# Kernel optimization log

Measured on AMD Instinct MI355X. Metric: run time of the kernel, lower is better.

The kernel has to match this reference:

```python
import jax, jax.numpy as jnp
import numpy as np


def setup_inputs() -> dict:
    key = jax.random.key(0)
    k1, k2 = jax.random.split(key)
    B, S_ENC, S_DEC, D = 8, 2048, 2048, 1024
    enc_outputs = jax.random.normal(k1, (B, S_ENC, D), dtype=jnp.float32)
    dec_outputs = jax.random.normal(k2, (B, S_DEC, D), dtype=jnp.float32)
    return {"enc_outputs": enc_outputs, "dec_outputs": dec_outputs}


def reference(enc_outputs, dec_outputs):
    # scores: [B, S_enc, S_dec] = enc @ dec^T (unscaled)
    a_t = jnp.einsum('bed,btd->bet', enc_outputs, dec_outputs)
    a_t = jax.nn.softmax(a_t, axis=-1)
    # context: [B, S_dec, D] = a_t^T @ enc
    c_t = jnp.einsum('bet,bed->btd', a_t, enc_outputs)
    return c_t
```

## Files before the change

### kernel.cpp

```cpp
#include <hip/hip_runtime.h>


typedef _Float16 half8 __attribute__((ext_vector_type(8)));
typedef _Float16 half4v __attribute__((ext_vector_type(4)));
typedef float floatx16 __attribute__((ext_vector_type(16)));

#define BM 128
#define BN 128
#define BK 32

__device__ __forceinline__ void async_load16(const _Float16* g, void* l) {
  __builtin_amdgcn_global_load_lds(
      (const __attribute__((address_space(1))) void*)g,
      (__attribute__((address_space(3))) void*)l, 16, 0, 0);
}

template <typename OutT, int RN>
__global__ __launch_bounds__(256, 2) void gemm_bt(
    const _Float16* __restrict__ A, const _Float16* __restrict__ Bt,
    OutT* __restrict__ C, int K, long strideA, long strideB, long strideC,
    int ldA, int ldB, int ldC) {
  __shared__ _Float16 lds_a[BM * BK];
  __shared__ _Float16 lds_b[BN * BK];

  const int b = blockIdx.z;
  A += (long)b * strideA;
  Bt += (long)b * strideB;
  C += (long)b * strideC;

  const int id = blockIdx.y * gridDim.x + blockIdx.x;
  const int xcd = id & 7;
  const int l = id >> 3;
  const int by = (xcd & 3) * 4 + l / RN;
  const int bx = (xcd >> 2) * RN + l % RN;
  const int m0 = by * BM;
  const int n0 = bx * BN;

  const int tid = threadIdx.x;
  const int lane = tid & 63;
  const int wave = tid >> 6;
  const int l31 = lane & 31;
  const int kh = lane >> 5;
  const int wm = (wave >> 1) * 64;
  const int wn = (wave & 1) * 64;

  floatx16 acc[2][2] = {};

  for (int k0 = 0; k0 < K; k0 += BK) {
#pragma unroll
    for (int c = 0; c < 2; ++c) {
      const int off = c * 4096 + wave * 1024 + lane * 16;
      const int row = off >> 6;
      const int ke = (((off >> 4) & 3) ^ (row & 3)) * 8;
      async_load16(A + (long)(m0 + row) * ldA + k0 + ke, (char*)lds_a + off);
      async_load16(Bt + (long)(n0 + row) * ldB + k0 + ke, (char*)lds_b + off);
    }
    __syncthreads();

    half8 af[2][2], bf[2][2];
#pragma unroll
    for (int i = 0; i < 2; ++i) {
      const int ra = wm + i * 32 + l31;
      const int rb = wn + i * 32 + l31;
#pragma unroll
      for (int s = 0; s < 2; ++s) {
        const int ck = s * 2 + kh;
        af[i][s] = *(const half8*)((const char*)lds_a + ra * 64 +
                                   ((ck ^ (ra & 3)) << 4));
        bf[i][s] = *(const half8*)((const char*)lds_b + rb * 64 +
                                   ((ck ^ (rb & 3)) << 4));
      }
    }
#pragma unroll
    for (int s = 0; s < 2; ++s)
#pragma unroll
      for (int i = 0; i < 2; ++i)
#pragma unroll
        for (int j = 0; j < 2; ++j)
          acc[i][j] = __builtin_amdgcn_mfma_f32_32x32x16_f16(
              af[i][s], bf[j][s], acc[i][j], 0, 0, 0);
    __syncthreads();
  }

#pragma unroll
  for (int i = 0; i < 2; ++i) {
    const int r_base = m0 + wm + i * 32 + 4 * kh;
#pragma unroll
    for (int j = 0; j < 2; ++j) {
      const int col = n0 + wn + j * 32 + l31;
#pragma unroll
      for (int g = 0; g < 4; ++g)
#pragma unroll
        for (int rr = 0; rr < 4; ++rr)
          C[(long)(r_base + g * 8 + rr) * ldC + col] =
              (OutT)acc[i][j][g * 4 + rr];
    }
  }
}

__global__ __launch_bounds__(256) void conv_enc(const float* __restrict__ E,
                                                _Float16* __restrict__ Eh,
                                                _Float16* __restrict__ EhT,
                                                int Se, int D) {
  __shared__ _Float16 T[64][72];
  const int b = blockIdx.z;
  const int d0 = blockIdx.x * 64;
  const int e0 = blockIdx.y * 64;
  const float* Eb = E + (size_t)b * Se * D;
  _Float16* Ehb = Eh + (size_t)b * Se * D;
  _Float16* EhTb = EhT + (size_t)b * D * Se;
  const int tid = threadIdx.x;
  const int tx = tid & 15;
  const int ty = tid >> 4;

  half4v h[4];
#pragma unroll
  for (int r = 0; r < 4; ++r) {
    const int e = e0 + ty * 4 + r;
    float4 v = *(const float4*)(Eb + (size_t)e * D + d0 + tx * 4);
    h[r][0] = (_Float16)v.x; h[r][1] = (_Float16)v.y;
    h[r][2] = (_Float16)v.z; h[r][3] = (_Float16)v.w;
    *(half4v*)(Ehb + (size_t)e * D + d0 + tx * 4) = h[r];
  }
#pragma unroll
  for (int c = 0; c < 4; ++c) {
    half4v w;
#pragma unroll
    for (int r = 0; r < 4; ++r) w[r] = h[r][c];
    *(half4v*)&T[tx * 4 + c][ty * 4] = w;
  }
  __syncthreads();
#pragma unroll
  for (int p = 0; p < 2; ++p) {
    const int idx = tid + p * 256;
    const int row = idx >> 3;
    const int ck = idx & 7;
    *(half8*)(EhTb + (size_t)(d0 + row) * Se + e0 + ck * 8) =
        *(const half8*)&T[row][ck * 8];
  }
}

__global__ __launch_bounds__(256) void conv_dec(const float* __restrict__ X,
                                                _Float16* __restrict__ Y) {
  const size_t i = ((size_t)blockIdx.x * 256 + threadIdx.x) * 8;
  float4 a = *(const float4*)(X + i);
  float4 b = *(const float4*)(X + i + 4);
  half8 h;
  h[0] = (_Float16)a.x; h[1] = (_Float16)a.y;
  h[2] = (_Float16)a.z; h[3] = (_Float16)a.w;
  h[4] = (_Float16)b.x; h[5] = (_Float16)b.y;
  h[6] = (_Float16)b.z; h[7] = (_Float16)b.w;
  *(half8*)(Y + i) = h;
}

__global__ __launch_bounds__(256) void row_stats(const _Float16* __restrict__ S,
                                                 float2* __restrict__ stats) {
  const int lane = threadIdx.x & 63;
  const long row = (long)blockIdx.x * 4 + (threadIdx.x >> 6);
  const _Float16* p = S + row * 2048;

  float f[32];
#pragma unroll
  for (int q = 0; q < 4; ++q) {
    half8 v = *(const half8*)(p + q * 512 + lane * 8);
#pragma unroll
    for (int j = 0; j < 8; ++j) f[q * 8 + j] = (float)v[j];
  }
  float mx = f[0];
#pragma unroll
  for (int j = 1; j < 32; ++j) mx = fmaxf(mx, f[j]);
  for (int o = 32; o; o >>= 1) mx = fmaxf(mx, __shfl_xor(mx, o, 64));
  float s = 0.f;
#pragma unroll
  for (int j = 0; j < 32; ++j) s += __expf(f[j] - mx);
  for (int o = 32; o; o >>= 1) s += __shfl_xor(s, o, 64);
  if (lane == 0) stats[row] = make_float2(mx, 1.0f / s);
}

__global__ __launch_bounds__(256) void norm_transpose(
    const _Float16* __restrict__ S, const float2* __restrict__ stats,
    _Float16* __restrict__ PT, int Se, int St) {
  __shared__ _Float16 T[64][72];
  const int b = blockIdx.z;
  const int t0 = blockIdx.x * 64;
  const int e0 = blockIdx.y * 64;
  const _Float16* Sb = S + (size_t)b * Se * St;
  _Float16* Pb = PT + (size_t)b * St * Se;
  const float2* stb = stats + (size_t)b * Se;
  const int tid = threadIdx.x;
  const int tx = tid & 15;
  const int ty = tid >> 4;

  half4v pr[4];
#pragma unroll
  for (int r = 0; r < 4; ++r) {
    const int e = e0 + ty * 4 + r;
    const float2 st = stb[e];
    half4v v = *(const half4v*)(Sb + (size_t)e * St + t0 + tx * 4);
#pragma unroll
    for (int c = 0; c < 4; ++c)
      pr[r][c] = (_Float16)(__expf((float)v[c] - st.x) * st.y);
  }
#pragma unroll
  for (int c = 0; c < 4; ++c) {
    half4v w;
#pragma unroll
    for (int r = 0; r < 4; ++r) w[r] = pr[r][c];
    *(half4v*)&T[tx * 4 + c][ty * 4] = w;
  }
  __syncthreads();
#pragma unroll
  for (int p = 0; p < 2; ++p) {
    const int idx = tid + p * 256;
    const int row = idx >> 3;
    const int ck = idx & 7;
    *(half8*)(Pb + (size_t)(t0 + row) * Se + e0 + ck * 8) =
        *(const half8*)&T[row][ck * 8];
  }
}

extern "C" void kernel_launch(void* const* d_in, const int* in_sizes, int n_in,
                              void* d_out, int out_size, void* d_ws,
                              size_t ws_size, hipStream_t stream) {
  const float* enc = (const float*)d_in[0];
  const float* dec = (const float*)d_in[1];
  float* out = (float*)d_out;

  const int B = 8, SE = 2048, SD = 2048, D = 1024;
  char* ws = (char*)d_ws;
  _Float16* enc_h = (_Float16*)ws;
  _Float16* dec_h = (_Float16*)(ws + 33554432);
  _Float16* PT = (_Float16*)ws;
  _Float16* enc_hT = (_Float16*)(ws + 67108864);
  _Float16* S_h = (_Float16*)(ws + 100663296);
  float2* stats = (float2*)(ws + 167772160);

  conv_enc<<<dim3(D / 64, SE / 64, B), 256, 0, stream>>>(enc, enc_h, enc_hT,
                                                         SE, D);
  conv_dec<<<dim3((size_t)B * SD * D / 2048), 256, 0, stream>>>(dec, dec_h);
  gemm_bt<_Float16, 8><<<dim3(SD / BN, SE / BM, B), 256, 0, stream>>>(
      enc_h, dec_h, S_h, D, (long)SE * D, (long)SD * D, (long)SE * SD, D, D,
      SD);
  row_stats<<<dim3(B * SE / 4), 256, 0, stream>>>(S_h, stats);
  norm_transpose<<<dim3(SD / 64, SE / 64, B), 256, 0, stream>>>(S_h, stats, PT,
                                                                SE, SD);
  gemm_bt<float, 4><<<dim3(D / BN, SD / BM, B), 256, 0, stream>>>(
      PT, enc_hT, out, SE, (long)SD * SE, (long)D * SE, (long)SD * D, SE, SE,
      D);
}
```

Baseline: 376.2 us.

## Emit transposed scores from GEMM epilogue, column-wise softmax stats, double GEMM BK

The first GEMM now writes the score matrix transposed through an LDS-staged epilogue, so the softmax normalization becomes a coalesced streaming pass instead of a separate transpose kernel. Softmax statistics are computed column-wise over the transposed layout with online max/sum partials, then merged in a small combine kernel. The GEMM K-tile grows from 32 to 64, halving loop iterations and barriers at the cost of more LDS per block, which may reduce occupancy. One extra kernel launch is added and the column-stat reads are narrower than the old row reads.

After: 349.9 us. 1.08x faster.

```diff
diff --git a/kernel.cpp b/kernel.cpp
--- a/kernel.cpp
+++ b/kernel.cpp
@@ -7,7 +7,7 @@
 
 #define BM 128
 #define BN 128
-#define BK 32
+#define BK 64
 
 __device__ __forceinline__ void async_load16(const _Float16* g, void* l) {
   __builtin_amdgcn_global_load_lds(
@@ -15,13 +15,16 @@
       (__attribute__((address_space(3))) void*)l, 16, 0, 0);
 }
 
-template <typename OutT, int RN>
+template <typename OutT, bool TRANS, int RN>
 __global__ __launch_bounds__(256, 2) void gemm_bt(
     const _Float16* __restrict__ A, const _Float16* __restrict__ Bt,
     OutT* __restrict__ C, int K, long strideA, long strideB, long strideC,
     int ldA, int ldB, int ldC) {
-  __shared__ _Float16 lds_a[BM * BK];
-  __shared__ _Float16 lds_b[BN * BK];
+  constexpr int CPR = BK / 8;
+  constexpr int SK = BK / 16;
+  __shared__ alignas(16) char smem[TRANS ? (128 * 136 * 2) : (2 * BM * BK * 2)];
+  _Float16* lds_a = (_Float16*)smem;
+  _Float16* lds_b = (_Float16*)(smem + BM * BK * 2);
 
   const int b = blockIdx.z;
   A += (long)b * strideA;
@@ -31,10 +34,8 @@
   const int id = blockIdx.y * gridDim.x + blockIdx.x;
   const int xcd = id & 7;
   const int l = id >> 3;
-  const int by = (xcd & 3) * 4 + l / RN;
-  const int bx = (xcd >> 2) * RN + l % RN;
-  const int m0 = by * BM;
-  const int n0 = bx * BN;
+  const int m0 = ((xcd & 3) * 4 + l / RN) * BM;
+  const int n0 = ((xcd >> 2) * RN + l % RN) * BN;
 
   const int tid = threadIdx.x;
   const int lane = tid & 63;
@@ -48,31 +49,31 @@
 
   for (int k0 = 0; k0 < K; k0 += BK) {
 #pragma unroll
-    for (int c = 0; c < 2; ++c) {
+    for (int c = 0; c < 4; ++c) {
       const int off = c * 4096 + wave * 1024 + lane * 16;
-      const int row = off >> 6;
-      const int ke = (((off >> 4) & 3) ^ (row & 3)) * 8;
+      const int row = off >> 7;
+      const int ke = (((off >> 4) & (CPR - 1)) ^ (row & (CPR - 1))) * 8;
       async_load16(A + (long)(m0 + row) * ldA + k0 + ke, (char*)lds_a + off);
       async_load16(Bt + (long)(n0 + row) * ldB + k0 + ke, (char*)lds_b + off);
     }
     __syncthreads();
 
-    half8 af[2][2], bf[2][2];
+    half8 af[2][SK], bf[2][SK];
 #pragma unroll
     for (int i = 0; i < 2; ++i) {
       const int ra = wm + i * 32 + l31;
       const int rb = wn + i * 32 + l31;
 #pragma unroll
-      for (int s = 0; s < 2; ++s) {
+      for (int s = 0; s < SK; ++s) {
         const int ck = s * 2 + kh;
-        af[i][s] = *(const half8*)((const char*)lds_a + ra * 64 +
-                                   ((ck ^ (ra & 3)) << 4));
-        bf[i][s] = *(const half8*)((const char*)lds_b + rb * 64 +
-                                   ((ck ^ (rb & 3)) << 4));
+        af[i][s] = *(const half8*)((const char*)lds_a + ra * (BK * 2) +
+                                   ((ck ^ (ra & (CPR - 1))) << 4));
+        bf[i][s] = *(const half8*)((const char*)lds_b + rb * (BK * 2) +
+                                   ((ck ^ (rb & (CPR - 1))) << 4));
       }
     }
 #pragma unroll
-    for (int s = 0; s < 2; ++s)
+    for (int s = 0; s < SK; ++s)
 #pragma unroll
       for (int i = 0; i < 2; ++i)
 #pragma unroll
@@ -82,18 +83,44 @@
     __syncthreads();
   }
 
-#pragma unroll
-  for (int i = 0; i < 2; ++i) {
-    const int r_base = m0 + wm + i * 32 + 4 * kh;
-#pragma unroll
-    for (int j = 0; j < 2; ++j) {
-      const int col = n0 + wn + j * 32 + l31;
-#pragma unroll
-      for (int g = 0; g < 4; ++g)
-#pragma unroll
-        for (int rr = 0; rr < 4; ++rr)
-          C[(long)(r_base + g * 8 + rr) * ldC + col] =
-              (OutT)acc[i][j][g * 4 + rr];
+  if constexpr (TRANS) {
+    _Float16(*TT)[136] = (_Float16(*)[136])smem;
+#pragma unroll
+    for (int i = 0; i < 2; ++i)
+#pragma unroll
+      for (int j = 0; j < 2; ++j) {
+        const int tl = wn + j * 32 + l31;
+#pragma unroll
+        for (int g = 0; g < 4; ++g) {
+          half4v h;
+#pragma unroll
+          for (int rr = 0; rr < 4; ++rr) h[rr] = (_Float16)acc[i][j][g * 4 + rr];
+          *(half4v*)&TT[tl][wm + i * 32 + 4 * kh + g * 8] = h;
+        }
+      }
+    __syncthreads();
+#pragma unroll
+    for (int p = 0; p < 8; ++p) {
+      const int idx = p * 256 + tid;
+      const int tl = idx >> 4;
+      const int ck = idx & 15;
+      *(half8*)((_Float16*)C + (long)(n0 + tl) * ldC + m0 + ck * 8) =
+          *(const half8*)&TT[tl][ck * 8];
+    }
+  } else {
+#pragma unroll
+    for (int i = 0; i < 2; ++i) {
+      const int r_base = m0 + wm + i * 32 + 4 * kh;
+#pragma unroll
+      for (int j = 0; j < 2; ++j) {
+        const int col = n0 + wn + j * 32 + l31;
+#pragma unroll
+        for (int g = 0; g < 4; ++g)
+#pragma unroll
+          for (int rr = 0; rr < 4; ++rr)
+            C[(long)(r_base + g * 8 + rr) * ldC + col] =
+                (OutT)acc[i][j][g * 4 + rr];
+      }
     }
   }
 }
@@ -153,69 +180,81 @@
   *(half8*)(Y + i) = h;
 }
 
-__global__ __launch_bounds__(256) void row_stats(const _Float16* __restrict__ S,
-                                                 float2* __restrict__ stats) {
-  const int lane = threadIdx.x & 63;
-  const long row = (long)blockIdx.x * 4 + (threadIdx.x >> 6);
-  const _Float16* p = S + row * 2048;
-
-  float f[32];
-#pragma unroll
-  for (int q = 0; q < 4; ++q) {
-    half8 v = *(const half8*)(p + q * 512 + lane * 8);
-#pragma unroll
-    for (int j = 0; j < 8; ++j) f[q * 8 + j] = (float)v[j];
-  }
-  float mx = f[0];
-#pragma unroll
-  for (int j = 1; j < 32; ++j) mx = fmaxf(mx, f[j]);
-  for (int o = 32; o; o >>= 1) mx = fmaxf(mx, __shfl_xor(mx, o, 64));
-  float s = 0.f;
-#pragma unroll
-  for (int j = 0; j < 32; ++j) s += __expf(f[j] - mx);
-  for (int o = 32; o; o >>= 1) s += __shfl_xor(s, o, 64);
-  if (lane == 0) stats[row] = make_float2(mx, 1.0f / s);
-}
-
-__global__ __launch_bounds__(256) void norm_transpose(
-    const _Float16* __restrict__ S, const float2* __restrict__ stats,
-    _Float16* __restrict__ PT, int Se, int St) {
-  __shared__ _Float16 T[64][72];
+__global__ __launch_bounds__(256) void col_stats(const _Float16* __restrict__ ST,
+                                                 float2* __restrict__ part) {
+  __shared__ float2 red[16][65];
   const int b = blockIdx.z;
-  const int t0 = blockIdx.x * 64;
-  const int e0 = blockIdx.y * 64;
-  const _Float16* Sb = S + (size_t)b * Se * St;
-  _Float16* Pb = PT + (size_t)b * St * Se;
-  const float2* stb = stats + (size_t)b * Se;
-  const int tid = threadIdx.x;
-  const int tx = tid & 15;
-  const int ty = tid >> 4;
-
-  half4v pr[4];
+  const int e0 = blockIdx.x * 64;
+  const int t0 = blockIdx.y * 512;
+  const _Float16* S = ST + (size_t)b * 2048 * 2048;
+  const int tx = threadIdx.x & 15;
+  const int ty = threadIdx.x >> 4;
+
+  float m[4] = {-1e30f, -1e30f, -1e30f, -1e30f};
+  float s[4] = {0.f, 0.f, 0.f, 0.f};
+  for (int it = 0; it < 32; ++it) {
+    const int t = t0 + it * 16 + ty;
+    half4v v = *(const half4v*)(S + (size_t)t * 2048 + e0 + tx * 4);
+#pragma unroll
+    for (int c = 0; c < 4; ++c) {
+      const float x = (float)v[c];
+      const float m2 = fmaxf(m[c], x);
+      s[c] = s[c] * __expf(m[c] - m2) + __expf(x - m2);
+      m[c] = m2;
+    }
+  }
+#pragma unroll
+  for (int c = 0; c < 4; ++c) red[ty][tx * 4 + c] = make_float2(m[c], s[c]);
+  __syncthreads();
+  if (threadIdx.x < 64) {
+    float2 a = red[0][threadIdx.x];
+#pragma unroll
+    for (int r = 1; r < 16; ++r) {
+      const float2 o = red[r][threadIdx.x];
+      const float m2 = fmaxf(a.x, o.x);
+      a.y = a.y * __expf(a.x - m2) + o.y * __expf(o.x - m2);
+      a.x = m2;
+    }
+    part[(size_t)blockIdx.y * 16384 + (size_t)b * 2048 + e0 + threadIdx.x] = a;
+  }
+}
+
+__global__ __launch_bounds__(256) void stats_combine(
+    const float2* __restrict__ part, float2* __restrict__ stats) {
+  const int idx = blockIdx.x * 256 + threadIdx.x;
+  float2 a = part[idx];
+#pragma unroll
+  for (int tc = 1; tc < 4; ++tc) {
+    const float2 o = part[tc * 16384 + idx];
+    const float m2 = fmaxf(a.x, o.x);
+    a.y = a.y * __expf(a.x - m2) + o.y * __expf(o.x - m2);
+    a.x = m2;
+  }
+  stats[idx] = make_float2(a.x, 1.0f / a.y);
+}
+
+__global__ __launch_bounds__(256) void norm_stream(
+    const _Float16* __restrict__ ST, const float2* __restrict__ stats,
+    _Float16* __restrict__ P) {
+  const int b = blockIdx.y;
+  const int t0 = blockIdx.x * 4;
+  const int e = threadIdx.x * 8;
+  float m_[8], rl_[8];
+#pragma unroll
+  for (int j = 0; j < 8; ++j) {
+    const float2 st = stats[(size_t)b * 2048 + e + j];
+    m_[j] = st.x;
+    rl_[j] = st.y;
+  }
+  const size_t base = ((size_t)b * 2048 + t0) * 2048 + e;
 #pragma unroll
   for (int r = 0; r < 4; ++r) {
-    const int e = e0 + ty * 4 + r;
-    const float2 st = stb[e];
-    half4v v = *(const half4v*)(Sb + (size_t)e * St + t0 + tx * 4);
-#pragma unroll
-    for (int c = 0; c < 4; ++c)
-      pr[r][c] = (_Float16)(__expf((float)v[c] - st.x) * st.y);
-  }
-#pragma unroll
-  for (int c = 0; c < 4; ++c) {
-    half4v w;
-#pragma unroll
-    for (int r = 0; r < 4; ++r) w[r] = pr[r][c];
-    *(half4v*)&T[tx * 4 + c][ty * 4] = w;
-  }
-  __syncthreads();
-#pragma unroll
-  for (int p = 0; p < 2; ++p) {
-    const int idx = tid + p * 256;
-    const int row = idx >> 3;
-    const int ck = idx & 7;
-    *(half8*)(Pb + (size_t)(t0 + row) * Se + e0 + ck * 8) =
-        *(const half8*)&T[row][ck * 8];
+    half8 v = *(const half8*)(ST + base + (size_t)r * 2048);
+    half8 o;
+#pragma unroll
+    for (int j = 0; j < 8; ++j)
+      o[j] = (_Float16)(__expf((float)v[j] - m_[j]) * rl_[j]);
+    *(half8*)(P + base + (size_t)r * 2048) = o;
   }
 }
 
@@ -230,21 +269,22 @@
   char* ws = (char*)d_ws;
   _Float16* enc_h = (_Float16*)ws;
   _Float16* dec_h = (_Float16*)(ws + 33554432);
-  _Float16* PT = (_Float16*)ws;
+  _Float16* P = (_Float16*)ws;
   _Float16* enc_hT = (_Float16*)(ws + 67108864);
-  _Float16* S_h = (_Float16*)(ws + 100663296);
+  _Float16* ST = (_Float16*)(ws + 100663296);
   float2* stats = (float2*)(ws + 167772160);
+  float2* part = (float2*)(ws + 167903232);
 
   conv_enc<<<dim3(D / 64, SE / 64, B), 256, 0, stream>>>(enc, enc_h, enc_hT,
                                                          SE, D);
   conv_dec<<<dim3((size_t)B * SD * D / 2048), 256, 0, stream>>>(dec, dec_h);
-  gemm_bt<_Float16, 8><<<dim3(SD / BN, SE / BM, B), 256, 0, stream>>>(
-      enc_h, dec_h, S_h, D, (long)SE * D, (long)SD * D, (long)SE * SD, D, D,
-      SD);
-  row_stats<<<dim3(B * SE / 4), 256, 0, stream>>>(S_h, stats);
-  norm_transpose<<<dim3(SD / 64, SE / 64, B), 256, 0, stream>>>(S_h, stats, PT,
-                                                                SE, SD);
-  gemm_bt<float, 4><<<dim3(D / BN, SD / BM, B), 256, 0, stream>>>(
-      PT, enc_hT, out, SE, (long)SD * SE, (long)D * SE, (long)SD * D, SE, SE,
+  gemm_bt<_Float16, true, 8><<<dim3(SD / BN, SE / BM, B), 256, 0, stream>>>(
+      enc_h, dec_h, ST, D, (long)SE * D, (long)SD * D, (long)SE * SD, D, D,
+      SE);
+  col_stats<<<dim3(32, 4, B), 256, 0, stream>>>(ST, part);
+  stats_combine<<<dim3(64), 256, 0, stream>>>(part, stats);
+  norm_stream<<<dim3(512, B), 256, 0, stream>>>(ST, stats, P);
+  gemm_bt<float, false, 4><<<dim3(D / BN, SD / BM, B), 256, 0, stream>>>(
+      P, enc_hT, out, SE, (long)SD * SE, (long)D * SE, (long)SD * D, SE, SE,
       D);
 }
```
